# Optimization experiments

Hardware: AMD Instinct MI355X
Metric: run time of the kernel (lower is better)

Reference implementation:

```python
import jax, jax.numpy as jnp
import numpy as np

D_MODEL, D_STATE, D_CONV, EXPAND = 1024, 16, 4, 2
D_INNER = EXPAND * D_MODEL
EPS = 1e-6


def setup_inputs() -> dict:
    key = jax.random.key(0)
    ks = jax.random.split(key, 8)
    B, T = 2, 1024
    s = lambda fan_in: 1.0 / np.sqrt(fan_in)
    x = jax.random.normal(ks[0], (B, T, D_MODEL), dtype=jnp.float32)
    norm_w = jnp.ones((D_MODEL,), jnp.float32)
    in_proj_w = jax.random.normal(ks[1], (D_MODEL, 2 * D_INNER), jnp.float32) * s(D_MODEL)
    conv_w = jax.random.normal(ks[2], (D_INNER, 1, D_CONV), jnp.float32) * s(D_CONV)
    dt_w = jax.random.normal(ks[3], (D_INNER, D_INNER), jnp.float32) * s(D_INNER)
    dt_b = jnp.zeros((D_INNER,), jnp.float32)
    # A_log init: log(arange(1..d_state)) repeated over d_inner rows
    A_log = jnp.log(jnp.broadcast_to(jnp.arange(1, D_STATE + 1, dtype=jnp.float32), (D_INNER, D_STATE)))
    B_w = jax.random.normal(ks[4], (D_INNER, D_STATE), jnp.float32) * s(D_INNER)
    C_w = jax.random.normal(ks[5], (D_INNER, D_STATE), jnp.float32) * s(D_INNER)
    D_skip = jnp.ones((D_INNER,), jnp.float32)
    out_proj_w = jax.random.normal(ks[6], (D_INNER, D_MODEL), jnp.float32) * s(D_INNER)
    return {"x": x, "norm_w": norm_w, "in_proj_w": in_proj_w, "conv_w": conv_w,
            "dt_w": dt_w, "dt_b": dt_b, "A_log": A_log, "B_w": B_w, "C_w": C_w,
            "D_skip": D_skip, "out_proj_w": out_proj_w}


def _forward(x, norm_w, in_proj_w, conv_w, dt_w, dt_b, A_log, B_w, C_w, D_skip, out_proj_w):
    Bsz, T, _ = x.shape
    # RMSNorm
    xn = x * jax.lax.rsqrt(jnp.mean(x * x, axis=-1, keepdims=True) + EPS) * norm_w
    # in_proj + gated silu
    xg = xn @ in_proj_w                                  # [B,T,2*di]
    x_inner, gate = jnp.split(xg, 2, axis=-1)
    x_inner = x_inner * jax.nn.silu(gate)                # [B,T,di]
    # causal depthwise conv (torch pads both sides then takes first T == left-pad only)
    xc = jax.lax.conv_general_dilated(
        x_inner.transpose(0, 2, 1), conv_w, window_strides=(1,),
        padding=[(D_CONV - 1, 0)], feature_group_count=D_INNER,
        dimension_numbers=("NCH", "OIH", "NCH")).transpose(0, 2, 1)  # [B,T,di]
    dt = jax.nn.softplus(xc @ dt_w + dt_b)               # [B,T,di]
    A = -jnp.exp(A_log)                                  # [di,ds]
    Bm = xc @ B_w                                        # [B,T,ds]
    Cm = xc @ C_w                                        # [B,T,ds]
    A_bar = jnp.exp(dt[..., None] * A)                   # [B,T,di,ds]
    B_bar = dt[..., None] * Bm[:, :, None, :]            # [B,T,di,ds]

    def step(h, inp):
        a_t, b_t, xc_t, c_t = inp                        # [B,di,ds],[B,di,ds],[B,di],[B,ds]
        h = a_t * h + b_t * xc_t[..., None]
        y = jnp.einsum("bds,bs->bd", h, c_t) + D_skip * xc_t
        return h, y

    h0 = jnp.zeros((Bsz, D_INNER, D_STATE), x.dtype)
    xs = (A_bar.transpose(1, 0, 2, 3), B_bar.transpose(1, 0, 2, 3),
          xc.transpose(1, 0, 2), Cm.transpose(1, 0, 2))
    _, ys = jax.lax.scan(step, h0, xs)                   # ys: [T,B,di]
    out = ys.transpose(1, 0, 2) @ out_proj_w             # [B,T,d_model]
    return out


def reference(x, norm_w, in_proj_w, conv_w, dt_w, dt_b, A_log, B_w, C_w, D_skip, out_proj_w):
    return _forward(x, norm_w, in_proj_w, conv_w, dt_w, dt_b, A_log, B_w, C_w, D_skip, out_proj_w)
```

## Files before the change

kernel.cpp:

```cpp
#include <hip/hip_runtime.h>
#include <cmath>


#define SEQ    1024
#define BATCH  2
#define DMODEL 1024
#define DINNER 2048
#define DSTATE 16
#define NTOK   (BATCH * SEQ)
#define NCHUNK 32
#define CLEN   32
#define NEXT   2112

typedef __attribute__((ext_vector_type(8))) short short8;
typedef __attribute__((ext_vector_type(4))) float f32x4;

__device__ __forceinline__ unsigned short f2bf(float f) {
  unsigned int u = __float_as_uint(f);
  unsigned int r = (u + 0x7fffu + ((u >> 16) & 1u)) >> 16;
  return (unsigned short)r;
}
__device__ __forceinline__ float bf2f(unsigned short v) {
  return __uint_as_float((unsigned int)v << 16);
}
__device__ __forceinline__ float softplus_f(float x) {
  return (x > 20.f) ? x : log1pf(__expf(x));
}
__device__ __forceinline__ void gload_lds16(const void* g, void* l) {
  __builtin_amdgcn_global_load_lds(
      (const __attribute__((address_space(1))) unsigned int*)g,
      (__attribute__((address_space(3))) unsigned int*)l, 16, 0, 0);
}

__device__ __forceinline__ size_t tiled_off(int row, int k, int kblks) {
  return ((size_t)(row >> 4) * kblks + (k >> 5)) * 512
       + ((size_t)((row & 15) + (((k >> 3) & 3) << 4)) << 3) + (k & 7);
}

__global__ __launch_bounds__(256) void init_aneg_k(const float* __restrict__ A_log,
                                                   float* __restrict__ Aneg) {
  int i = blockIdx.x * 256 + threadIdx.x;
  Aneg[i] = -__expf(A_log[i]);
}

__global__ void transpose_cvt_k(const float* __restrict__ W, unsigned short* __restrict__ Wt,
                                int K, int N) {
  __shared__ float tile[32][33];
  int k0 = blockIdx.y * 32, n0 = blockIdx.x * 32;
  int tx = threadIdx.x, ty = threadIdx.y;
  int kblks = K >> 5;
#pragma unroll
  for (int i = 0; i < 32; i += 8)
    tile[ty + i][tx] = W[(size_t)(k0 + ty + i) * N + n0 + tx];
  __syncthreads();
#pragma unroll
  for (int i = 0; i < 32; i += 8)
    Wt[tiled_off(n0 + ty + i, k0 + tx, kblks)] = f2bf(tile[tx][ty + i]);
}

__global__ void build_w2t_k(const float* __restrict__ dt_w, const float* __restrict__ B_w,
                            const float* __restrict__ C_w, unsigned short* __restrict__ Wt) {
  __shared__ float tile[32][33];
  int k0 = blockIdx.x * 32, n0 = blockIdx.y * 32;
  int tx = threadIdx.x, ty = threadIdx.y;
  if (n0 < DINNER) {
#pragma unroll
    for (int i = 0; i < 32; i += 8)
      tile[ty + i][tx] = dt_w[(size_t)(k0 + ty + i) * DINNER + n0 + tx];
    __syncthreads();
#pragma unroll
    for (int i = 0; i < 32; i += 8)
      Wt[tiled_off(n0 + ty + i, k0 + tx, 64)] = f2bf(tile[tx][ty + i]);
  } else {
#pragma unroll
    for (int i = 0; i < 32; i += 8) {
      int n = n0 + ty + i;
      float v = 0.f;
      if (n < DINNER + 16) v = B_w[(size_t)(k0 + tx) * DSTATE + (n - DINNER)];
      else if (n < DINNER + 32) v = C_w[(size_t)(k0 + tx) * DSTATE + (n - DINNER - 16)];
      Wt[tiled_off(n, k0 + tx, 64)] = f2bf(v);
    }
  }
}

__global__ __launch_bounds__(256) void rmsnorm_k(const float* __restrict__ x,
                                                 const float* __restrict__ w,
                                                 unsigned short* __restrict__ xnbf) {
  int row = blockIdx.x, tid = threadIdx.x;
  const float4 v = *(const float4*)(x + (size_t)row * DMODEL + tid * 4);
  float ss = v.x * v.x + v.y * v.y + v.z * v.z + v.w * v.w;
#pragma unroll
  for (int off = 32; off > 0; off >>= 1) ss += __shfl_down(ss, off);
  __shared__ float red[4];
  if ((tid & 63) == 0) red[tid >> 6] = ss;
  __syncthreads();
  float tot = red[0] + red[1] + red[2] + red[3];
  float scale = rsqrtf(tot * (1.0f / DMODEL) + 1e-6f);
  const float4 wv = *(const float4*)(w + tid * 4);
  ushort4 o;
  o.x = f2bf(v.x * scale * wv.x);
  o.y = f2bf(v.y * scale * wv.y);
  o.z = f2bf(v.z * scale * wv.z);
  o.w = f2bf(v.w * scale * wv.w);
  *(ushort4*)(xnbf + tiled_off(row, tid * 4, DMODEL / 32)) = o;
}

template <int BM, int BN, int MODE>
__global__ __launch_bounds__(256) void gemm_bf16_t(const unsigned short* __restrict__ At,
                                                   const unsigned short* __restrict__ Btt,
                                                   float* __restrict__ C,
                                                   int M, int N, int K, int ldc,
                                                   const float* __restrict__ bias,
                                                   float* __restrict__ Bm,
                                                   float* __restrict__ Cm) {
  constexpr int WTM = BM / 2, WTN = BN / 2;
  constexpr int FM = WTM / 16, FN = WTN / 16;
  constexpr int ASUB = BM / 16, BSUB = BN / 16;
  constexpr int ALOAD = ASUB * 2, BLOAD = BSUB * 2;
  __shared__ __align__(16) unsigned short Abuf[2][BM * 64];
  __shared__ __align__(16) unsigned short Bbuf[2][BN * 64];
  const int tid = threadIdx.x;
  const int wave = tid >> 6, lane = tid & 63;

  const int gx = gridDim.x;
  int lin = blockIdx.y * gx + blockIdx.x;
  int nwg = gx * gridDim.y;
  int swz = (lin & 7) * (nwg >> 3) + (lin >> 3);
  const int bm = (swz / gx) * BM, bn = (swz % gx) * BN;

  const int wm = wave >> 1, wn = wave & 1;
  const int kblks = K >> 5;
  const unsigned short* Ag = At + ((size_t)(bm >> 4) * kblks) * 512 + (lane << 3);
  const unsigned short* Bg = Btt + ((size_t)(bn >> 4) * kblks) * 512 + (lane << 3);

  auto stage = [&](int buf, int t) {
#pragma unroll
    for (int i = wave; i < ALOAD; i += 4) {
      int s = i >> 1, kk = i & 1;
      gload_lds16(Ag + ((size_t)s * kblks + 2 * t + kk) * 512,
                  &Abuf[buf][(kk * ASUB + s) * 512]);
    }
#pragma unroll
    for (int i = wave; i < BLOAD; i += 4) {
      int s = i >> 1, kk = i & 1;
      gload_lds16(Bg + ((size_t)s * kblks + 2 * t + kk) * 512,
                  &Bbuf[buf][(kk * BSUB + s) * 512]);
    }
  };

  f32x4 acc[FM][FN] = {};
  const int nt = K / 64;
  stage(0, 0);
  __syncthreads();
  int cur = 0;
  for (int t = 0; t < nt; ++t) {
    if (t + 1 < nt) stage(cur ^ 1, t + 1);
#pragma unroll
    for (int kk = 0; kk < 2; ++kk) {
      short8 af[FM], bfr[FN];
#pragma unroll
      for (int m = 0; m < FM; ++m)
        af[m] = *(const short8*)&Abuf[cur][(kk * ASUB + wm * FM + m) * 512 + (lane << 3)];
#pragma unroll
      for (int n = 0; n < FN; ++n)
        bfr[n] = *(const short8*)&Bbuf[cur][(kk * BSUB + wn * FN + n) * 512 + (lane << 3)];
#pragma unroll
      for (int m = 0; m < FM; ++m)
#pragma unroll
        for (int n = 0; n < FN; ++n)
          acc[m][n] = __builtin_amdgcn_mfma_f32_16x16x32_bf16(af[m], bfr[n], acc[m][n], 0, 0, 0);
    }
    __syncthreads();
    cur ^= 1;
  }

  const int rbase = bm + wm * WTM + (lane >> 4) * 4;
  const int cbase = bn + wn * WTN + (lane & 15);
#pragma unroll
  for (int m = 0; m < FM; ++m)
#pragma unroll
    for (int n = 0; n < FN; ++n) {
      int col = cbase + n * 16;
#pragma unroll
      for (int r = 0; r < 4; ++r) {
        int row = rbase + m * 16 + r;
        float v = acc[m][n][r];
        if (MODE == 0) {
          C[(size_t)row * ldc + col] = v;
        } else {
          if (col < DINNER)
            C[(size_t)row * DINNER + col] = softplus_f(v + bias[col]);
          else if (col < DINNER + 16)
            Bm[(size_t)row * DSTATE + (col - DINNER)] = v;
          else if (col < DINNER + 32)
            Cm[(size_t)row * DSTATE + (col - DINNER - 16)] = v;
        }
      }
    }
}

__global__ __launch_bounds__(256) void siluconv_k(const float* __restrict__ xg,
                                                  const float* __restrict__ w,
                                                  unsigned short* __restrict__ xcbf) {
  int idx = blockIdx.x * 256 + threadIdx.x;
  int d4 = (idx & 511) << 2;
  int tc = (idx >> 9) & 127;
  int b = idx >> 16;
  float4 w0 = *(const float4*)(w + (d4 + 0) * 4);
  float4 w1 = *(const float4*)(w + (d4 + 1) * 4);
  float4 w2 = *(const float4*)(w + (d4 + 2) * 4);
  float4 w3 = *(const float4*)(w + (d4 + 3) * 4);
  const float wj0[4] = {w0.x, w0.y, w0.z, w0.w};
  const float wj1[4] = {w1.x, w1.y, w1.z, w1.w};
  const float wj2[4] = {w2.x, w2.y, w2.z, w2.w};
  const float wj3[4] = {w3.x, w3.y, w3.z, w3.w};
  const float* pa = xg + (size_t)b * SEQ * (2 * DINNER) + d4;
  const float* pg = pa + DINNER;
  int t0 = tc * 8;
  float4 sA = {0.f, 0.f, 0.f, 0.f}, sB = sA, sC = sA;
  auto gated = [&](int t) {
    float4 a = *(const float4*)(pa + (size_t)t * (2 * DINNER));
    float4 g = *(const float4*)(pg + (size_t)t * (2 * DINNER));
    float4 r;
    r.x = a.x * (g.x / (1.f + __expf(-g.x)));
    r.y = a.y * (g.y / (1.f + __expf(-g.y)));
    r.z = a.z * (g.z / (1.f + __expf(-g.z)));
    r.w = a.w * (g.w / (1.f + __expf(-g.w)));
    return r;
  };
  if (t0 > 0) {
    sA = gated(t0 - 3);
    sB = gated(t0 - 2);
    sC = gated(t0 - 1);
  }
#pragma unroll
  for (int j = 0; j < 8; ++j) {
    int t = t0 + j;
    float4 sD = gated(t);
    float4 o;
    o.x = sA.x * wj0[0] + sB.x * wj0[1] + sC.x * wj0[2] + sD.x * wj0[3];
    o.y = sA.y * wj1[0] + sB.y * wj1[1] + sC.y * wj1[2] + sD.y * wj1[3];
    o.z = sA.z * wj2[0] + sB.z * wj2[1] + sC.z * wj2[2] + sD.z * wj2[3];
    o.w = sA.w * wj3[0] + sB.w * wj3[1] + sC.w * wj3[2] + sD.w * wj3[3];
    ushort4 ob = {f2bf(o.x), f2bf(o.y), f2bf(o.z), f2bf(o.w)};
    *(ushort4*)(xcbf + tiled_off(b * SEQ + t, d4, 64)) = ob;
    sA = sB; sB = sC; sC = sD;
  }
}

__global__ __launch_bounds__(256) void scan_local_k(const float* __restrict__ dt,
                                                    const unsigned short* __restrict__ xcbf,
                                                    const float* __restrict__ Bm,
                                                    const float* __restrict__ A,
                                                    float* __restrict__ hfin,
                                                    float* __restrict__ P) {
  int d = blockIdx.x * 256 + threadIdx.x;
  int c = blockIdx.y, b = blockIdx.z;
  float a[DSTATE], h[DSTATE];
#pragma unroll
  for (int s = 0; s < DSTATE; ++s) { a[s] = A[(size_t)d * DSTATE + s]; h[s] = 0.f; }
  float sdt = 0.f;
  int t0 = c * CLEN;
  for (int t = t0; t < t0 + CLEN; ++t) {
    size_t ro = (size_t)(b * SEQ + t);
    float dtv = dt[ro * DINNER + d];
    float xv = bf2f(xcbf[tiled_off((int)ro, d, 64)]);
    sdt += dtv;
    float bx = dtv * xv;
    float4 q0 = *(const float4*)(Bm + ro * DSTATE + 0);
    float4 q1 = *(const float4*)(Bm + ro * DSTATE + 4);
    float4 q2 = *(const float4*)(Bm + ro * DSTATE + 8);
    float4 q3 = *(const float4*)(Bm + ro * DSTATE + 12);
    float bm[DSTATE] = {q0.x, q0.y, q0.z, q0.w, q1.x, q1.y, q1.z, q1.w,
                        q2.x, q2.y, q2.z, q2.w, q3.x, q3.y, q3.z, q3.w};
#pragma unroll
    for (int s = 0; s < DSTATE; ++s) {
      float av = __expf(a[s] * dtv);
      h[s] = fmaf(av, h[s], bx * bm[s]);
    }
  }
  size_t o = ((size_t)(b * NCHUNK + c) * DINNER + d) * DSTATE;
#pragma unroll
  for (int s = 0; s < DSTATE; ++s) {
    hfin[o + s] = h[s];
    P[o + s] = __expf(a[s] * sdt);
  }
}

__global__ __launch_bounds__(256) void scan_chunks_k(float* hp, const float* __restrict__ P) {
  int j = blockIdx.x * 256 + threadIdx.x;
  int b = j / (DINNER * DSTATE);
  int r = j % (DINNER * DSTATE);
  float H = 0.f;
  for (int c = 0; c < NCHUNK; ++c) {
    size_t o = ((size_t)(b * NCHUNK + c) * DINNER * DSTATE) + r;
    float hf = hp[o];
    float pv = P[o];
    hp[o] = H;
    H = fmaf(pv, H, hf);
  }
}

__global__ __launch_bounds__(256) void scan_final_k(const float* __restrict__ dt,
                                                    const unsigned short* __restrict__ xcbf,
                                                    const float* __restrict__ Bm,
                                                    const float* __restrict__ Cm,
                                                    const float* __restrict__ A,
                                                    const float* __restrict__ Hprev,
                                                    const float* __restrict__ Dskip,
                                                    unsigned short* __restrict__ ysbf) {
  int d = blockIdx.x * 256 + threadIdx.x;
  int c = blockIdx.y, b = blockIdx.z;
  float a[DSTATE], h[DSTATE];
  size_t ho = ((size_t)(b * NCHUNK + c) * DINNER + d) * DSTATE;
#pragma unroll
  for (int s = 0; s < DSTATE; ++s) {
    a[s] = A[(size_t)d * DSTATE + s];
    h[s] = Hprev[ho + s];
  }
  float Dv = Dskip[d];
  int t0 = c * CLEN;
  for (int t = t0; t < t0 + CLEN; ++t) {
    size_t ro = (size_t)(b * SEQ + t);
    float dtv = dt[ro * DINNER + d];
    float xv = bf2f(xcbf[tiled_off((int)ro, d, 64)]);
    float bx = dtv * xv;
    float4 q0 = *(const float4*)(Bm + ro * DSTATE + 0);
    float4 q1 = *(const float4*)(Bm + ro * DSTATE + 4);
    float4 q2 = *(const float4*)(Bm + ro * DSTATE + 8);
    float4 q3 = *(const float4*)(Bm + ro * DSTATE + 12);
    float bm[DSTATE] = {q0.x, q0.y, q0.z, q0.w, q1.x, q1.y, q1.z, q1.w,
                        q2.x, q2.y, q2.z, q2.w, q3.x, q3.y, q3.z, q3.w};
    float4 r0 = *(const float4*)(Cm + ro * DSTATE + 0);
    float4 r1 = *(const float4*)(Cm + ro * DSTATE + 4);
    float4 r2 = *(const float4*)(Cm + ro * DSTATE + 8);
    float4 r3 = *(const float4*)(Cm + ro * DSTATE + 12);
    float cm[DSTATE] = {r0.x, r0.y, r0.z, r0.w, r1.x, r1.y, r1.z, r1.w,
                        r2.x, r2.y, r2.z, r2.w, r3.x, r3.y, r3.z, r3.w};
    float y = Dv * xv;
#pragma unroll
    for (int s = 0; s < DSTATE; ++s) {
      float av = __expf(a[s] * dtv);
      h[s] = fmaf(av, h[s], bx * bm[s]);
      y = fmaf(h[s], cm[s], y);
    }
    ysbf[tiled_off((int)ro, d, 64)] = f2bf(y);
  }
}

extern "C" void kernel_launch(void* const* d_in, const int* in_sizes, int n_in,
                              void* d_out, int out_size, void* d_ws, size_t ws_size,
                              hipStream_t stream) {
  (void)in_sizes; (void)n_in; (void)out_size; (void)ws_size;
  const float* x       = (const float*)d_in[0];
  const float* norm_w  = (const float*)d_in[1];
  const float* in_proj = (const float*)d_in[2];
  const float* conv_w  = (const float*)d_in[3];
  const float* dt_w    = (const float*)d_in[4];
  const float* dt_b    = (const float*)d_in[5];
  const float* A_log   = (const float*)d_in[6];
  const float* B_w     = (const float*)d_in[7];
  const float* C_w     = (const float*)d_in[8];
  const float* D_skip  = (const float*)d_in[9];
  const float* out_w   = (const float*)d_in[10];
  float* out = (float*)d_out;
  float* ws = (float*)d_ws;

  float* Aneg = ws;
  float* Bm   = ws + 32768;
  float* Cm   = ws + 65536;
  float* b0   = ws + 98304;
  float* xg   = b0;
  float* dtb  = b0;
  float* hfin = b0 + 4194304;
  float* Pbuf = b0 + 6291456;
  unsigned short* xc_bf = (unsigned short*)(b0 + 8388608);
  unsigned short* ys_bf = (unsigned short*)(b0 + 10485760);
  float* Rw   = b0 + 12582912;
  unsigned short* in_wT  = (unsigned short*)Rw;
  unsigned short* W2t    = (unsigned short*)Rw;
  unsigned short* out_wT = (unsigned short*)Rw;
  unsigned short* xn_bf  = (unsigned short*)(b0 + 14745600);

  init_aneg_k<<<dim3(DINNER * DSTATE / 256), dim3(256), 0, stream>>>(A_log, Aneg);
  transpose_cvt_k<<<dim3(2 * DINNER / 32, DMODEL / 32), dim3(32, 8), 0, stream>>>(
      in_proj, in_wT, DMODEL, 2 * DINNER);
  rmsnorm_k<<<dim3(NTOK), dim3(256), 0, stream>>>(x, norm_w, xn_bf);
  gemm_bf16_t<128, 128, 0><<<dim3(2 * DINNER / 128, NTOK / 128), dim3(256), 0, stream>>>(
      xn_bf, in_wT, xg, NTOK, 2 * DINNER, DMODEL, 2 * DINNER, nullptr, nullptr, nullptr);
  siluconv_k<<<dim3(NTOK * (DINNER / 4) / 8 / 256), dim3(256), 0, stream>>>(
      xg, conv_w, xc_bf);
  build_w2t_k<<<dim3(DINNER / 32, NEXT / 32), dim3(32, 8), 0, stream>>>(
      dt_w, B_w, C_w, W2t);
  gemm_bf16_t<128, 64, 2><<<dim3(NEXT / 64, NTOK / 128), dim3(256), 0, stream>>>(
      xc_bf, W2t, dtb, NTOK, NEXT, DINNER, DINNER, dt_b, Bm, Cm);
  scan_local_k<<<dim3(DINNER / 256, NCHUNK, BATCH), dim3(256), 0, stream>>>(
      dtb, xc_bf, Bm, Aneg, hfin, Pbuf);
  scan_chunks_k<<<dim3(BATCH * DINNER * DSTATE / 256), dim3(256), 0, stream>>>(
      hfin, Pbuf);
  scan_final_k<<<dim3(DINNER / 256, NCHUNK, BATCH), dim3(256), 0, stream>>>(
      dtb, xc_bf, Bm, Cm, Aneg, hfin, D_skip, ys_bf);
  transpose_cvt_k<<<dim3(DMODEL / 32, DINNER / 32), dim3(32, 8), 0, stream>>>(
      out_w, out_wT, DINNER, DMODEL);
  gemm_bf16_t<64, 64, 0><<<dim3(DMODEL / 64, NTOK / 64), dim3(256), 0, stream>>>(
      ys_bf, out_wT, out, NTOK, DMODEL, DINNER, DMODEL, nullptr, nullptr, nullptr);
}
```

Measured before the change: 184.8 us.

## Deepen GEMM global-to-LDS prefetch to two stages with vmcnt-based waits

Restructures the bf16 GEMM main loop so two K tiles are in flight. Each wave waits only until its older batch of direct-to-LDS loads has landed (partial vmcnt), reads all fragments into registers, then issues the load for tile t+2 into the freed buffer before running the MFMAs. This aims to hide global load latency behind compute instead of blocking at a full __syncthreads each iteration. In exchange it holds more fragment registers, and correctness depends on the hand-computed per-wave load count matching the vmcnt value.

```diff
diff --git a/kernel.cpp b/kernel.cpp
--- a/kernel.cpp
+++ b/kernel.cpp
@@ -30,6 +30,14 @@
   __builtin_amdgcn_global_load_lds(
       (const __attribute__((address_space(1))) unsigned int*)g,
       (__attribute__((address_space(3))) unsigned int*)l, 16, 0, 0);
+}
+
+template <int N>
+__device__ __forceinline__ void wait_vmcnt() {
+  if constexpr (N >= 8)      asm volatile("s_waitcnt vmcnt(8)" ::: "memory");
+  else if constexpr (N == 6) asm volatile("s_waitcnt vmcnt(6)" ::: "memory");
+  else if constexpr (N == 4) asm volatile("s_waitcnt vmcnt(4)" ::: "memory");
+  else                       asm volatile("s_waitcnt vmcnt(0)" ::: "memory");
 }
 
 __device__ __forceinline__ size_t tiled_off(int row, int k, int kblks) {
@@ -117,6 +125,7 @@
   constexpr int FM = WTM / 16, FN = WTN / 16;
   constexpr int ASUB = BM / 16, BSUB = BN / 16;
   constexpr int ALOAD = ASUB * 2, BLOAD = BSUB * 2;
+  constexpr int LPW = (BM + BN) / 32;
   __shared__ __align__(16) unsigned short Abuf[2][BM * 64];
   __shared__ __align__(16) unsigned short Bbuf[2][BN * 64];
   const int tid = threadIdx.x;
@@ -151,27 +160,34 @@
   f32x4 acc[FM][FN] = {};
   const int nt = K / 64;
   stage(0, 0);
-  __syncthreads();
-  int cur = 0;
+  stage(1, 1);
   for (int t = 0; t < nt; ++t) {
-    if (t + 1 < nt) stage(cur ^ 1, t + 1);
+    const int cur = t & 1;
+    if (t + 1 < nt) wait_vmcnt<LPW>();
+    else            wait_vmcnt<0>();
+    __builtin_amdgcn_s_barrier();
+    short8 af[2][FM], bfr[2][FN];
 #pragma unroll
     for (int kk = 0; kk < 2; ++kk) {
-      short8 af[FM], bfr[FN];
 #pragma unroll
       for (int m = 0; m < FM; ++m)
-        af[m] = *(const short8*)&Abuf[cur][(kk * ASUB + wm * FM + m) * 512 + (lane << 3)];
+        af[kk][m] = *(const short8*)&Abuf[cur][(kk * ASUB + wm * FM + m) * 512 + (lane << 3)];
 #pragma unroll
       for (int n = 0; n < FN; ++n)
-        bfr[n] = *(const short8*)&Bbuf[cur][(kk * BSUB + wn * FN + n) * 512 + (lane << 3)];
+        bfr[kk][n] = *(const short8*)&Bbuf[cur][(kk * BSUB + wn * FN + n) * 512 + (lane << 3)];
+    }
+    asm volatile("s_waitcnt lgkmcnt(0)" ::: "memory");
+    __builtin_amdgcn_sched_barrier(0);
+    __builtin_amdgcn_s_barrier();
+    if (t + 2 < nt) stage(cur, t + 2);
+#pragma unroll
+    for (int kk = 0; kk < 2; ++kk)
 #pragma unroll
       for (int m = 0; m < FM; ++m)
 #pragma unroll
         for (int n = 0; n < FN; ++n)
-          acc[m][n] = __builtin_amdgcn_mfma_f32_16x16x32_bf16(af[m], bfr[n], acc[m][n], 0, 0, 0);
-    }
-    __syncthreads();
-    cur ^= 1;
+          acc[m][n] = __builtin_amdgcn_mfma_f32_16x16x32_bf16(af[kk][m], bfr[kk][n],
+                                                              acc[m][n], 0, 0, 0);
   }
 
   const int rbase = bm + wm * WTM + (lane >> 4) * 4;
```

Measured after the change: 178.7 us. 1.03x faster.
